# Performance work log

Hardware: AMD Instinct MI355X
Metric: run time of the kernel (lower is better)

The kernel has to match this reference:

```python
import jax, jax.numpy as jnp
import numpy as np

B, N, D = 4, 1024, 1024
T_ITER = 4
E_TYPES = 4  # edge_type_num; module loops over E_TYPES+1 with bitmask
ALPHA = 0.2


def _lin_w(key, out_f, in_f):
    # fan-avg uniform init from custom Linear
    bound = float(np.sqrt(3.0 / ((in_f + out_f) / 2.0)))
    return jax.random.uniform(key, (out_f, in_f), minval=-bound, maxval=bound, dtype=jnp.float32)


def setup_inputs() -> dict:
    key = jax.random.key(0)
    ks = jax.random.split(key, 32)
    inp = {}
    inp['ents'] = jax.random.normal(ks[0], (B, N, D), jnp.float32)
    inp['ent_mask'] = jnp.ones((B, N), jnp.float32)
    inp['q_encoding'] = jax.random.normal(ks[1], (B, D), jnp.float32)
    inp['adj'] = jax.random.randint(ks[2], (B, N, N), 0, E_TYPES + 1, dtype=jnp.int32)
    inp['types'] = 30  # bits 1..4 set -> edge types 1..4 active
    inp['init_mem'] = jax.random.normal(ks[3], (1, D), jnp.float32)
    inp['w_qin'] = _lin_w(ks[4], D, D); inp['b_qin'] = jnp.zeros((D,), jnp.float32)
    inp['w_qt'] = jnp.stack([_lin_w(ks[5 + t], D, D) for t in range(T_ITER)])
    inp['b_qt'] = jnp.zeros((T_ITER, D), jnp.float32)
    inp['w_pl'] = _lin_w(ks[9], D, D);  inp['b_pl'] = jnp.zeros((D,), jnp.float32)
    inp['w_pc'] = _lin_w(ks[10], D, D); inp['b_pc'] = jnp.zeros((D,), jnp.float32)
    inp['w_q'] = _lin_w(ks[11], D, 3 * D); inp['b_q'] = jnp.zeros((D,), jnp.float32)
    inp['w_k'] = _lin_w(ks[12], D, 3 * D); inp['b_k'] = jnp.zeros((D,), jnp.float32)
    inp['w_v'] = _lin_w(ks[13], D, 3 * D); inp['b_v'] = jnp.zeros((D,), jnp.float32)
    inp['w_pk'] = _lin_w(ks[14], D, D); inp['b_pk'] = jnp.zeros((D,), jnp.float32)
    inp['w_pv'] = _lin_w(ks[15], D, D); inp['b_pv'] = jnp.zeros((D,), jnp.float32)
    # wes: xavier_uniform(gain=1.414) on shape (2D, 1); stored flat as (E_TYPES, 2D)
    wb = 1.414 * float(np.sqrt(6.0 / (2 * D + 1)))
    inp['wes'] = jax.random.uniform(ks[16], (E_TYPES, 2 * D), minval=-wb, maxval=wb, dtype=jnp.float32)
    inp['w_mu'] = _lin_w(ks[17], D, 2 * D); inp['b_mu'] = jnp.zeros((D,), jnp.float32)
    inp['w_cb'] = _lin_w(ks[18], D, 2 * D); inp['b_cb'] = jnp.zeros((D,), jnp.float32)
    return inp


def _lin(x, w, b):
    return x @ w.T + b


def _qdgat_forward(ents, ent_mask, q_encoding, adj, types, init_mem,
                   w_qin, b_qin, w_qt, b_qt, w_pl, b_pl, w_pc, b_pc,
                   w_q, b_q, w_k, b_k, w_v, b_v, w_pk, b_pk, w_pv, b_pv,
                   wes, w_mu, b_mu, w_cb, b_cb):
    d = ents.shape[-1]
    x_loc = ents
    x_ctx = jnp.broadcast_to(init_mem, ents.shape)
    # eval mode: var-drop mask is ones scaled by ent_mask
    var_drop = ent_mask[:, :, None]
    adj_pos = adj > 0
    q_base = jax.nn.elu(_lin(q_encoding, w_qin, b_qin))
    n_types = wes.shape[0] + 1  # self.edge_type_num = edge_type_num + 1
    for t in range(T_ITER):
        cmd = _lin(q_base, w_qt[t], b_qt[t])                      # [B,D]
        xc = x_ctx * var_drop
        pl = _lin(x_loc, w_pl, b_pl)
        pc = _lin(xc, w_pc, b_pc)
        x_joint = jnp.concatenate([x_loc, xc, pl * pc], axis=-1)   # [B,N,3D]
        q = _lin(x_joint, w_q, b_q)                               # [B,N,D]
        k = _lin(x_joint, w_k, b_k) * _lin(cmd, w_pk, b_pk)[:, None, :]
        v = _lin(x_joint, w_v, b_v) * _lin(cmd, w_pv, b_pv)[:, None, :]
        # edge_score[b,i,j] = sum over active types T of (adj==T) * (q_i . we[:D] + k_j . we[D:])
        # equivalent to matmul((cat(q_i,k_j) * (adj==T)), we) without materializing [B,N,N,2D]
        edge_score = jnp.zeros(adj.shape, jnp.float32)
        for i in range(n_types):
            if (types >> i) & 1 == 1:
                w1, w2 = wes[i - 1, :d], wes[i - 1, d:]  # i=0 aliases wes[-1], as in torch
                s = (q @ w1)[:, :, None] + (k @ w2)[:, None, :]    # [B,N,N]
                edge_score = edge_score + jnp.where(adj == i, s, 0.0)
        e = jnp.where(edge_score > 0, edge_score, ALPHA * edge_score)  # leaky relu
        logits = jnp.where(adj_pos, e, jnp.float32(-9e15))
        prob = jax.nn.softmax(logits, axis=-1)                     # [B,N,N]
        message = jnp.einsum('bij,bjd->bid', prob, v)
        x_ctx = _lin(jnp.concatenate([xc, message], axis=-1), w_mu, b_mu)
    return _lin(jnp.concatenate([x_loc, x_ctx], axis=-1), w_cb, b_cb)


def reference(ents, ent_mask, q_encoding, adj, types, init_mem,
              w_qin, b_qin, w_qt, b_qt, w_pl, b_pl, w_pc, b_pc,
              w_q, b_q, w_k, b_k, w_v, b_v, w_pk, b_pk, w_pv, b_pv,
              wes, w_mu, b_mu, w_cb, b_cb):
    return _qdgat_forward(ents, ent_mask, q_encoding, adj, types, init_mem,
                          w_qin, b_qin, w_qt, b_qt, w_pl, b_pl, w_pc, b_pc,
                          w_q, b_q, w_k, b_k, w_v, b_v, w_pk, b_pk, w_pv, b_pv,
                          wes, w_mu, b_mu, w_cb, b_cb)
```

## Files before the change

kernel.cpp:

```cpp
#include <hip/hip_runtime.h>
#include <hip/hip_bf16.h>
#include <stdint.h>
#include <stddef.h>


typedef __hip_bfloat16 bf16;
typedef __attribute__((ext_vector_type(8))) short short8;
typedef __attribute__((ext_vector_type(4))) float floatx4;

#define NB 4
#define NN 1024
#define DD 1024
#define NT_ITER 4
#define MM (NB * NN)

static __device__ __forceinline__ float b2f(bf16 x) { return __bfloat162float(x); }
static __device__ __forceinline__ bf16 f2b(float x) { return __float2bfloat16(x); }
static __device__ __forceinline__ unsigned short f2bu(float x) {
    bf16 h = __float2bfloat16(x);
    unsigned short u;
    __builtin_memcpy(&u, &h, 2);
    return u;
}
static __device__ __forceinline__ float bu2f(unsigned short u) {
    unsigned int t = (unsigned int)u << 16;
    float f;
    __builtin_memcpy(&f, &t, 4);
    return f;
}

static __device__ __forceinline__ void gl_lds16(const void* g, void* l) {
    __builtin_amdgcn_global_load_lds(
        (const __attribute__((address_space(1))) unsigned int*)g,
        (__attribute__((address_space(3))) unsigned int*)l, 16, 0, 0);
}

template <int N>
static __device__ __forceinline__ void s_wait_vmcnt() {
    if constexpr (N == 0)      asm volatile("s_waitcnt vmcnt(0)" ::: "memory");
    else if constexpr (N == 4) asm volatile("s_waitcnt vmcnt(4)" ::: "memory");
    else if constexpr (N == 6) asm volatile("s_waitcnt vmcnt(6)" ::: "memory");
    else if constexpr (N == 8) asm volatile("s_waitcnt vmcnt(8)" ::: "memory");
}

__global__ void k_f2b(const float* __restrict__ src, bf16* __restrict__ dst, int n4) {
    int i = blockIdx.x * 256 + threadIdx.x;
    if (i >= n4) return;
    float4 v = ((const float4*)src)[i];
    ushort4 o;
    o.x = f2bu(v.x); o.y = f2bu(v.y); o.z = f2bu(v.z); o.w = f2bu(v.w);
    ((ushort4*)dst)[i] = o;
}

__global__ void k_transw(const float* __restrict__ src, bf16* __restrict__ dst) {
    __shared__ float tile[32][33];
    int c0 = blockIdx.x * 32;
    int r0 = blockIdx.y * 32;
    int tx = threadIdx.x, ty = threadIdx.y;
    for (int i = 0; i < 32; i += 8)
        tile[ty + i][tx] = src[(size_t)(r0 + ty + i) * 3072 + c0 + tx];
    __syncthreads();
    for (int i = 0; i < 32; i += 8)
        dst[(size_t)(c0 + ty + i) * 1024 + r0 + tx] = f2b(tile[tx][ty + i]);
}

__global__ void k_build_sc(const float* __restrict__ pk, const float* __restrict__ wes,
                           bf16* __restrict__ Aq, bf16* __restrict__ Ak) {
    int i = blockIdx.x * 256 + threadIdx.x;
    int half = i >> 16;
    int j = i & 65535;
    int row = j >> 10, d = j & 1023;
    if (half == 0) {
        Aq[j] = (row < 4) ? f2b(wes[(size_t)row * 2048 + d]) : f2b(0.f);
    } else {
        int t = row >> 4, b = (row >> 2) & 3, e = row & 3;
        Ak[j] = f2b(pk[((size_t)t * NB + b) * DD + d] * wes[(size_t)e * 2048 + 1024 + d]);
    }
}

__global__ __launch_bounds__(256) void k_qbase(const float* __restrict__ qenc, const float* __restrict__ w,
                                               const float* __restrict__ b, float* __restrict__ out) {
    int o = blockIdx.x * 4 + (threadIdx.x >> 6);
    int lane = threadIdx.x & 63;
    int n = o >> 2, r = o & 3;
    const float* xr = qenc + (size_t)r * DD;
    const float* wr = w + (size_t)n * DD;
    float s = 0.f;
    for (int d = lane; d < DD; d += 64) s += xr[d] * wr[d];
    for (int off = 32; off; off >>= 1) s += __shfl_down(s, off);
    if (lane == 0) {
        s += b[n];
        out[(size_t)r * DD + n] = s > 0.f ? s : (expf(s) - 1.0f);
    }
}

__global__ __launch_bounds__(256) void k_cmd(const float* __restrict__ qb, const float* __restrict__ w_qt,
                                             const float* __restrict__ b_qt, float* __restrict__ cmd) {
    int o = blockIdx.x * 4 + (threadIdx.x >> 6);
    int lane = threadIdx.x & 63;
    int r = o & 3, n = (o >> 2) & 1023, t = o >> 12;
    const float* xr = qb + (size_t)r * DD;
    const float* wr = w_qt + ((size_t)t * DD + n) * DD;
    float s = 0.f;
    for (int d = lane; d < DD; d += 64) s += xr[d] * wr[d];
    for (int off = 32; off; off >>= 1) s += __shfl_down(s, off);
    if (lane == 0) cmd[((size_t)t * NB + r) * DD + n] = s + b_qt[t * DD + n];
}

__global__ __launch_bounds__(256) void k_pkpv(const float* __restrict__ cmd,
                                              const float* __restrict__ w_pk, const float* __restrict__ b_pk,
                                              const float* __restrict__ w_pv, const float* __restrict__ b_pv,
                                              float* __restrict__ pk, float* __restrict__ pv) {
    int o = blockIdx.x * 4 + (threadIdx.x >> 6);
    int lane = threadIdx.x & 63;
    int n = o >> 5, half = (o >> 4) & 1, pair = o & 15;
    const float* xr = cmd + (size_t)pair * DD;
    const float* wr = (half ? w_pv : w_pk) + (size_t)n * DD;
    float s = 0.f;
    for (int d = lane; d < DD; d += 64) s += xr[d] * wr[d];
    for (int off = 32; off; off >>= 1) s += __shfl_down(s, off);
    if (lane == 0)
        (half ? pv : pk)[(size_t)pair * DD + n] = s + (half ? b_pv : b_pk)[n];
}

__global__ void k_consts(const float* __restrict__ b_q, const float* __restrict__ b_k,
                         const float* __restrict__ pk, const float* __restrict__ wes,
                         float* __restrict__ cq, float* __restrict__ ck) {
    int o = blockIdx.x;
    int lane = threadIdx.x;
    float s = 0.f;
    if (o < 4) {
        for (int d = lane; d < 1024; d += 64) s += b_q[d] * wes[(size_t)o * 2048 + d];
    } else {
        int oo = o - 4;
        int t = oo >> 4, b = (oo >> 2) & 3, e = oo & 3;
        for (int d = lane; d < 1024; d += 64)
            s += b_k[d] * pk[((size_t)t * NB + b) * DD + d] * wes[(size_t)e * 2048 + 1024 + d];
    }
    for (int off = 32; off; off >>= 1) s += __shfl_down(s, off);
    if (lane == 0) {
        if (o < 4) cq[o] = s;
        else ck[o - 4] = s;
    }
}

__global__ __launch_bounds__(256) void k_qakb2(const bf16* __restrict__ ents, const bf16* __restrict__ xc,
                                               const bf16* __restrict__ plpc,
                                               const float* __restrict__ wqtw, const float* __restrict__ wkeff_t,
                                               const float* __restrict__ cq, const float* __restrict__ ck_t,
                                               float* __restrict__ qa, float* __restrict__ kb) {
    __shared__ float red[4][8];
    int m = blockIdx.x;
    int b = m >> 10;
    int t = threadIdx.x;
    float aq[4] = {0.f, 0.f, 0.f, 0.f}, ak[4] = {0.f, 0.f, 0.f, 0.f};
    const bf16* rows[3] = {ents + (size_t)m * DD, xc + (size_t)m * DD, plpc + (size_t)m * DD};
#pragma unroll
    for (int c = 0; c < 3; ++c) {
        const bf16* row = rows[c];
        const float* wq = wqtw + c * 1024;
        const float* wk = wkeff_t + (size_t)b * 4 * 3072 + c * 1024;
        for (int d = t; d < 1024; d += 256) {
            float xv = b2f(row[d]);
#pragma unroll
            for (int e = 0; e < 4; ++e) {
                aq[e] += xv * wq[(size_t)e * 3072 + d];
                ak[e] += xv * wk[(size_t)e * 3072 + d];
            }
        }
    }
#pragma unroll
    for (int e = 0; e < 4; ++e) {
        float v = aq[e];
        for (int o = 32; o; o >>= 1) v += __shfl_down(v, o);
        if ((t & 63) == 0) red[t >> 6][e] = v;
        v = ak[e];
        for (int o = 32; o; o >>= 1) v += __shfl_down(v, o);
        if ((t & 63) == 0) red[t >> 6][e + 4] = v;
    }
    __syncthreads();
    if (t < 8) {
        float s = red[0][t] + red[1][t] + red[2][t] + red[3][t];
        if (t < 4) qa[(size_t)m * 4 + t] = s + cq[t];
        else kb[(size_t)m * 4 + (t - 4)] = s + ck_t[b * 4 + (t - 4)];
    }
}

__global__ void k_init(const bf16* __restrict__ initm_bf, const float* __restrict__ mask,
                       bf16* __restrict__ x_ctx, bf16* __restrict__ xc) {
    int i = blockIdx.x * 256 + threadIdx.x;
    uint4 v = ((const uint4*)initm_bf)[i & 127];
    ((uint4*)x_ctx)[i] = v;
    float mk = mask[i >> 7];
    unsigned short* u = (unsigned short*)&v;
#pragma unroll
    for (int j = 0; j < 8; ++j) u[j] = f2bu(bu2f(u[j]) * mk);
    ((uint4*)xc)[i] = v;
}

template <int WM, int WN>
__device__ __forceinline__ void gemm_core(
    const bf16* __restrict__ A0, const bf16* __restrict__ A1, const bf16* __restrict__ A2,
    const bf16* __restrict__ W, const float* __restrict__ bias, void* __restrict__ C,
    const void* __restrict__ mul, const float* __restrict__ addC, bf16* __restrict__ C2,
    int mulmode, int storef32, int nchunks, int ldw, int ldc,
    int bm, int bn) {
    constexpr int BM = WM * 2;
    constexpr int BN = WN * 2;
    constexpr int MI = WM / 16;
    constexpr int NI = WN / 16;
    constexpr int SEGS = (BM + BN) / 8;
    constexpr int SPW = SEGS / 4;
    __shared__ bf16 sAB[3][(BM + BN) * 64];

    const int t = threadIdx.x;
    const int lane = t & 63;
    const int w = t >> 6;
    const int wm = (w & 1) * WM, wn = (w >> 1) * WN;
    const int srow = lane >> 3;
    const int scol = ((lane & 7) * 8) ^ (srow << 3);

    floatx4 acc[MI][NI];
#pragma unroll
    for (int i = 0; i < MI; ++i)
#pragma unroll
        for (int j = 0; j < NI; ++j) acc[i][j] = (floatx4){0.f, 0.f, 0.f, 0.f};

    const int lrow = lane & 15;
    const int kq = (lane >> 4) * 8;
    const int kx = (lane & 7) << 3;
    const int ktiles = nchunks * 16;

    auto stage = [&](int buf, int kt) {
        const int cidx = kt >> 4;
        const bf16* Ac = (cidx == 0) ? A0 : (cidx == 1 ? A1 : A2);
        const int klocal = (kt & 15) * 64;
        const int kglob = kt * 64;
#pragma unroll
        for (int s = 0; s < SPW; ++s) {
            int c = w * SPW + s;
            if (c < BM / 8) {
                const bf16* src = Ac + ((size_t)(bm * BM + c * 8 + srow)) * 1024 + klocal + scol;
                gl_lds16(src, &sAB[buf][c * 512]);
            } else {
                const bf16* src = W + ((size_t)(bn * BN + (c - BM / 8) * 8 + srow)) * (size_t)ldw + kglob + scol;
                gl_lds16(src, &sAB[buf][c * 512]);
            }
        }
    };

    stage(0, 0);
    if (ktiles > 1) stage(1, 1);
    int cur = 0, sb = 2;
    for (int kt = 0; kt < ktiles; ++kt) {
        if (kt + 1 < ktiles) s_wait_vmcnt<SPW>();
        else s_wait_vmcnt<0>();
        __builtin_amdgcn_s_barrier();
        __builtin_amdgcn_sched_barrier(0);
        short8 af[2][MI], bfr[2][NI];
#pragma unroll
        for (int ks = 0; ks < 2; ++ks) {
            const int ko = (ks * 32 + kq) ^ kx;
#pragma unroll
            for (int mi = 0; mi < MI; ++mi)
                af[ks][mi] = *(const short8*)&sAB[cur][(wm + mi * 16 + lrow) * 64 + ko];
#pragma unroll
            for (int ni = 0; ni < NI; ++ni)
                bfr[ks][ni] = *(const short8*)&sAB[cur][BM * 64 + (wn + ni * 16 + lrow) * 64 + ko];
        }
        if (kt + 2 < ktiles) stage(sb, kt + 2);
        __builtin_amdgcn_s_setprio(1);
#pragma unroll
        for (int ks = 0; ks < 2; ++ks)
#pragma unroll
            for (int mi = 0; mi < MI; ++mi)
#pragma unroll
                for (int ni = 0; ni < NI; ++ni)
                    acc[mi][ni] = __builtin_amdgcn_mfma_f32_16x16x32_bf16(af[ks][mi], bfr[ks][ni], acc[mi][ni], 0, 0, 0);
        __builtin_amdgcn_s_setprio(0);
        asm volatile("s_waitcnt lgkmcnt(0)" ::: "memory");
        __builtin_amdgcn_sched_barrier(0);
        cur = (cur == 2) ? 0 : cur + 1;
        sb = (sb == 2) ? 0 : sb + 1;
    }

    const int qrow = (lane >> 4) * 4;
#pragma unroll
    for (int mi = 0; mi < MI; ++mi) {
#pragma unroll
        for (int ni = 0; ni < NI; ++ni) {
            int gn = bn * BN + wn + ni * 16 + lrow;
            float bv = bias ? bias[gn] : 0.f;
#pragma unroll
            for (int r = 0; r < 4; ++r) {
                int gm = bm * BM + wm + mi * 16 + qrow + r;
                size_t ci = (size_t)gm * (size_t)ldc + gn;
                float val = acc[mi][ni][r] + bv;
                if (addC) val += addC[ci];
                if (mulmode == 1)
                    val *= b2f(((const bf16*)mul)[(size_t)gm * 1024 + gn]);
                else if (mulmode == 2)
                    val *= ((const float*)mul)[(size_t)(gm >> 10) * 1024 + gn];
                if (storef32) {
                    ((float*)C)[ci] = val;
                } else {
                    ((bf16*)C)[ci] = f2b(val);
                    if (mulmode == 3)
                        C2[ci] = f2b(val * ((const float*)mul)[gm]);
                }
            }
        }
    }
}

template <int WM, int WN>
__global__ __launch_bounds__(256) void k_gemm_t(
    const bf16* __restrict__ A0, const bf16* __restrict__ A1, const bf16* __restrict__ A2,
    const bf16* __restrict__ W, const float* __restrict__ bias, void* __restrict__ C,
    const void* __restrict__ mul, const float* __restrict__ addC, bf16* __restrict__ C2,
    int mulmode, int storef32, int nchunks, int ldw, int ldc,
    long long sA, long long sW, long long sC) {
    int bz = blockIdx.z;
    const bf16* A0b = A0 + (size_t)bz * sA;
    const bf16* Wb = W + (size_t)bz * sW;
    void* Cb = storef32 ? (void*)((float*)C + (size_t)bz * sC)
                        : (void*)((bf16*)C + (size_t)bz * sC);
    gemm_core<WM, WN>(A0b, A1, A2, Wb, bias, Cb, mul, addC, C2, mulmode, storef32, nchunks, ldw, ldc,
                      blockIdx.x, blockIdx.y);
}

__global__ void k_transpose(const bf16* __restrict__ v, bf16* __restrict__ vT) {
    __shared__ bf16 tile[32][33];
    int b = blockIdx.z;
    int n0 = blockIdx.x * 32, d0 = blockIdx.y * 32;
    int tx = threadIdx.x, ty = threadIdx.y;
    for (int i = 0; i < 32; i += 8)
        tile[ty + i][tx] = v[((size_t)b * NN + n0 + ty + i) * DD + d0 + tx];
    __syncthreads();
    for (int i = 0; i < 32; i += 8)
        vT[((size_t)b * DD + d0 + ty + i) * NN + n0 + tx] = tile[tx][ty + i];
}

__global__ __launch_bounds__(256) void k_attn(const int* __restrict__ adj, const float* __restrict__ qa,
                                              const float* __restrict__ kb, const int* __restrict__ typesPtr,
                                              bf16* __restrict__ prob) {
    __shared__ float lg[NN];
    __shared__ float red[4];
    __shared__ float red2[4];
    int m = blockIdx.x;
    int b = m >> 10;
    int t = threadIdx.x;
    int types = typesPtr[0];
    float qa4[4];
#pragma unroll
    for (int e = 0; e < 4; ++e) qa4[e] = qa[(size_t)m * 4 + e];
    const int* arow = adj + (size_t)m * NN;
    const float* kbb = kb + (size_t)(b << 10) * 4;

    float lmax = -3.0e38f;
    for (int j = t; j < NN; j += 256) {
        int a = arow[j];
        float l;
        if (a == 0) {
            l = -9.0e15f;
        } else if ((types >> a) & 1) {
            float s = qa4[a - 1] + kbb[(size_t)j * 4 + (a - 1)];
            l = s > 0.f ? s : 0.2f * s;
        } else {
            l = 0.f;
        }
        lg[j] = l;
        lmax = fmaxf(lmax, l);
    }
    for (int o = 32; o > 0; o >>= 1) lmax = fmaxf(lmax, __shfl_down(lmax, o));
    if ((t & 63) == 0) red[t >> 6] = lmax;
    __syncthreads();
    lmax = fmaxf(fmaxf(red[0], red[1]), fmaxf(red[2], red[3]));

    float lsum = 0.f;
    for (int j = t; j < NN; j += 256) {
        float ex = __expf(lg[j] - lmax);
        lg[j] = ex;
        lsum += ex;
    }
    for (int o = 32; o > 0; o >>= 1) lsum += __shfl_down(lsum, o);
    if ((t & 63) == 0) red2[t >> 6] = lsum;
    __syncthreads();
    lsum = red2[0] + red2[1] + red2[2] + red2[3];
    float inv = 1.0f / lsum;

    bf16* prow = prob + (size_t)m * NN;
    for (int j = t; j < NN; j += 256) prow[j] = f2b(lg[j] * inv);
}

extern "C" void kernel_launch(void* const* d_in, const int* in_sizes, int n_in,
                              void* d_out, int out_size, void* d_ws, size_t ws_size,
                              hipStream_t stream) {
    const float* ents = (const float*)d_in[0];
    const float* mask = (const float*)d_in[1];
    const float* qenc = (const float*)d_in[2];
    const int* adj = (const int*)d_in[3];
    const int* types = (const int*)d_in[4];
    const float* initm = (const float*)d_in[5];
    const float* w_qin = (const float*)d_in[6];
    const float* b_qin = (const float*)d_in[7];
    const float* w_qt = (const float*)d_in[8];
    const float* b_qt = (const float*)d_in[9];
    const float* w_pl = (const float*)d_in[10];
    const float* b_pl = (const float*)d_in[11];
    const float* w_pc = (const float*)d_in[12];
    const float* b_pc = (const float*)d_in[13];
    const float* w_q = (const float*)d_in[14];
    const float* b_q = (const float*)d_in[15];
    const float* w_k = (const float*)d_in[16];
    const float* b_k = (const float*)d_in[17];
    const float* w_v = (const float*)d_in[18];
    const float* b_v = (const float*)d_in[19];
    const float* w_pk = (const float*)d_in[20];
    const float* b_pk = (const float*)d_in[21];
    const float* w_pv = (const float*)d_in[22];
    const float* b_pv = (const float*)d_in[23];
    const float* wes = (const float*)d_in[24];
    const float* w_mu = (const float*)d_in[25];
    const float* b_mu = (const float*)d_in[26];
    const float* w_cb = (const float*)d_in[27];
    const float* b_cb = (const float*)d_in[28];
    (void)in_sizes; (void)n_in; (void)out_size; (void)ws_size;

    char* p = (char*)d_ws;
    auto carve = [&](size_t bytes) {
        char* r = p;
        p += (bytes + 255) & ~(size_t)255;
        return r;
    };
    float* q_base = (float*)carve((size_t)NB * DD * 4);
    float* cmd = (float*)carve((size_t)NT_ITER * NB * DD * 4);
    float* pk = (float*)carve((size_t)NT_ITER * NB * DD * 4);
    float* pv = (float*)carve((size_t)NT_ITER * NB * DD * 4);
    float* qa = (float*)carve((size_t)MM * 4 * 4);
    float* kb = (float*)carve((size_t)MM * 4 * 4);
    float* wqtw = (float*)carve((size_t)64 * 3072 * 4);
    float* wkeff = (float*)carve((size_t)64 * 3072 * 4);
    float* cq = (float*)carve(4 * 4);
    float* ck = (float*)carve(64 * 4);
    float* vent = (float*)carve((size_t)MM * DD * 4);
    bf16* initm_bf = (bf16*)carve((size_t)DD * 2);
    bf16* ents_bf = (bf16*)carve((size_t)MM * DD * 2);
    bf16* wpl_bf = (bf16*)carve((size_t)DD * DD * 2);
    bf16* wpc_bf = (bf16*)carve((size_t)DD * DD * 2);
    bf16* wv_bf = (bf16*)carve((size_t)DD * 3 * DD * 2);
    bf16* wmu_bf = (bf16*)carve((size_t)DD * 2 * DD * 2);
    bf16* wcb_bf = (bf16*)carve((size_t)DD * 2 * DD * 2);
    bf16* wqT_bf = (bf16*)carve((size_t)3 * DD * DD * 2);
    bf16* wkT_bf = (bf16*)carve((size_t)3 * DD * DD * 2);
    bf16* Aq = (bf16*)carve((size_t)64 * DD * 2);
    bf16* Ak = (bf16*)carve((size_t)64 * DD * 2);
    bf16* x_ctx = (bf16*)carve((size_t)MM * DD * 2);
    bf16* xc = (bf16*)carve((size_t)MM * DD * 2);
    bf16* pl = (bf16*)carve((size_t)MM * DD * 2);
    bf16* plpc = (bf16*)carve((size_t)MM * DD * 2);
    bf16* vbuf = (bf16*)carve((size_t)MM * DD * 2);
    bf16* msg = (bf16*)carve((size_t)MM * DD * 2);
    bf16* prob = (bf16*)carve((size_t)NB * NN * NN * 2);
    bf16* vT = plpc;

    const dim3 blk(256);
    const dim3 g128(32, 8, 1);
    const dim3 gMsg(8, 8, NB);
    const dim3 gPre(1, 48, 1);

    k_f2b<<<1, blk, 0, stream>>>(initm, initm_bf, DD / 4);
    k_f2b<<<4096, blk, 0, stream>>>(ents, ents_bf, MM * DD / 4);
    k_f2b<<<1024, blk, 0, stream>>>(w_pl, wpl_bf, DD * DD / 4);
    k_f2b<<<1024, blk, 0, stream>>>(w_pc, wpc_bf, DD * DD / 4);
    k_f2b<<<3072, blk, 0, stream>>>(w_v, wv_bf, DD * 3 * DD / 4);
    k_f2b<<<2048, blk, 0, stream>>>(w_mu, wmu_bf, DD * 2 * DD / 4);
    k_f2b<<<2048, blk, 0, stream>>>(w_cb, wcb_bf, DD * 2 * DD / 4);
    k_transw<<<dim3(96, 32), dim3(32, 8), 0, stream>>>(w_q, wqT_bf);
    k_transw<<<dim3(96, 32), dim3(32, 8), 0, stream>>>(w_k, wkT_bf);

    k_qbase<<<1024, blk, 0, stream>>>(qenc, w_qin, b_qin, q_base);
    k_cmd<<<4096, blk, 0, stream>>>(q_base, w_qt, b_qt, cmd);
    k_pkpv<<<8192, blk, 0, stream>>>(cmd, w_pk, b_pk, w_pv, b_pv, pk, pv);
    k_init<<<2048, blk, 0, stream>>>(initm_bf, mask, x_ctx, xc);

    k_build_sc<<<512, blk, 0, stream>>>(pk, wes, Aq, Ak);
    k_consts<<<68, 64, 0, stream>>>(b_q, b_k, pk, wes, cq, ck);
    k_gemm_t<32, 32><<<gPre, blk, 0, stream>>>(Aq, nullptr, nullptr, wqT_bf, nullptr, wqtw,
                                               nullptr, nullptr, nullptr, 0, 1, 1, 1024, 3072, 0, 0, 0);
    k_gemm_t<32, 32><<<gPre, blk, 0, stream>>>(Ak, nullptr, nullptr, wkT_bf, nullptr, wkeff,
                                               nullptr, nullptr, nullptr, 0, 1, 1, 1024, 3072, 0, 0, 0);

    k_gemm_t<64, 64><<<g128, blk, 0, stream>>>(ents_bf, nullptr, nullptr, wpl_bf, b_pl, pl,
                                               nullptr, nullptr, nullptr, 0, 0, 1, 1024, 1024, 0, 0, 0);
    k_gemm_t<64, 64><<<g128, blk, 0, stream>>>(ents_bf, nullptr, nullptr, wv_bf, nullptr, vent,
                                               nullptr, nullptr, nullptr, 0, 1, 1, 3072, 1024, 0, 0, 0);

    for (int t = 0; t < NT_ITER; ++t) {
        k_gemm_t<64, 64><<<g128, blk, 0, stream>>>(xc, nullptr, nullptr, wpc_bf, b_pc, plpc,
                                                   pl, nullptr, nullptr, 1, 0, 1, 1024, 1024, 0, 0, 0);
        k_gemm_t<64, 64><<<g128, blk, 0, stream>>>(xc, plpc, nullptr, wv_bf + 1024, b_v, vbuf,
                                                   pv + (size_t)t * NB * DD, vent, nullptr, 2, 0, 2, 3072, 1024, 0, 0, 0);
        k_qakb2<<<4096, blk, 0, stream>>>(ents_bf, xc, plpc,
                                          wqtw, wkeff + (size_t)t * 16 * 3072,
                                          cq, ck + t * 16, qa, kb);
        k_transpose<<<dim3(32, 32, NB), dim3(32, 8), 0, stream>>>(vbuf, vT);
        k_attn<<<4096, blk, 0, stream>>>(adj, qa, kb, types, prob);
        k_gemm_t<64, 64><<<gMsg, blk, 0, stream>>>(prob, nullptr, nullptr, vT, nullptr, msg,
                                                   nullptr, nullptr, nullptr, 0, 0, 1, 1024, 1024,
                                                   (long long)NN * NN, (long long)DD * NN, (long long)NN * DD);
        k_gemm_t<64, 64><<<g128, blk, 0, stream>>>(xc, msg, nullptr, wmu_bf, b_mu, x_ctx,
                                                   mask, nullptr, xc, 3, 0, 2, 2048, 1024, 0, 0, 0);
    }
    k_gemm_t<64, 64><<<g128, blk, 0, stream>>>(ents_bf, x_ctx, nullptr, wcb_bf, b_cb, (float*)d_out,
                                               nullptr, nullptr, nullptr, 0, 1, 2, 2048, 1024, 0, 0, 0);
}
```

Before: 1.075 ms.

## Replace LDS-tiled GEMM with direct global-to-register double-buffered MFMA GEMM

```diff
diff --git a/kernel.cpp b/kernel.cpp
--- a/kernel.cpp
+++ b/kernel.cpp
@@ -196,6 +196,104 @@
 #pragma unroll
     for (int j = 0; j < 8; ++j) u[j] = f2bu(bu2f(u[j]) * mk);
     ((uint4*)xc)[i] = v;
+}
+
+struct Frags {
+    short8 a[8];
+    short8 b[8];
+};
+
+__global__ __launch_bounds__(256, 1) void k_gemm_d(
+    const bf16* __restrict__ A0, const bf16* __restrict__ A1, const bf16* __restrict__ A2,
+    const bf16* __restrict__ W, const float* __restrict__ bias, void* __restrict__ C,
+    const void* __restrict__ mul, const float* __restrict__ addC, bf16* __restrict__ C2,
+    int mulmode, int storef32, int nchunks, int ldw, int ldc,
+    long long sA, long long sW, long long sC) {
+    const int bz = blockIdx.z;
+    const bf16* A0b = A0 + (size_t)bz * sA;
+    const bf16* Wb = W + (size_t)bz * sW;
+
+    const int t = threadIdx.x;
+    const int lane = t & 63;
+    const int w = t >> 6;
+    const int lrow = lane & 15;
+    const int kq = (lane >> 4) * 8;
+    const int arow = blockIdx.x * 128 + (w & 1) * 64 + lrow;
+    const int wrow = blockIdx.y * 128 + (w >> 1) * 64 + lrow;
+    const int ktiles = nchunks * 16;
+
+    floatx4 acc[4][4];
+#pragma unroll
+    for (int i = 0; i < 4; ++i)
+#pragma unroll
+        for (int j = 0; j < 4; ++j) acc[i][j] = (floatx4){0.f, 0.f, 0.f, 0.f};
+
+    auto loadF = [&](Frags& f, int kt) {
+        const int cidx = kt >> 4;
+        const bf16* Ac = (cidx == 0) ? A0b : (cidx == 1 ? A1 : A2);
+        const bf16* Ab = Ac + (size_t)arow * 1024 + (kt & 15) * 64 + kq;
+        const bf16* Wp = Wb + (size_t)wrow * (size_t)ldw + (size_t)kt * 64 + kq;
+#pragma unroll
+        for (int ks = 0; ks < 2; ++ks) {
+#pragma unroll
+            for (int mi = 0; mi < 4; ++mi)
+                f.a[ks * 4 + mi] = *(const short8*)(Ab + (size_t)mi * 16 * 1024 + ks * 32);
+#pragma unroll
+            for (int ni = 0; ni < 4; ++ni)
+                f.b[ks * 4 + ni] = *(const short8*)(Wp + (size_t)ni * 16 * (size_t)ldw + ks * 32);
+        }
+    };
+    auto mfmaF = [&](const Frags& f) {
+#pragma unroll
+        for (int ks = 0; ks < 2; ++ks)
+#pragma unroll
+            for (int mi = 0; mi < 4; ++mi)
+#pragma unroll
+                for (int ni = 0; ni < 4; ++ni)
+                    acc[mi][ni] = __builtin_amdgcn_mfma_f32_16x16x32_bf16(
+                        f.a[ks * 4 + mi], f.b[ks * 4 + ni], acc[mi][ni], 0, 0, 0);
+    };
+
+    Frags f0, f1;
+    loadF(f0, 0);
+    loadF(f1, 1);
+    int kt = 0;
+    for (; kt < ktiles - 2; kt += 2) {
+        mfmaF(f0);
+        loadF(f0, kt + 2);
+        mfmaF(f1);
+        loadF(f1, kt + 3);
+    }
+    mfmaF(f0);
+    mfmaF(f1);
+
+    const int qrow = (lane >> 4) * 4;
+#pragma unroll
+    for (int mi = 0; mi < 4; ++mi) {
+#pragma unroll
+        for (int ni = 0; ni < 4; ++ni) {
+            int gn = blockIdx.y * 128 + (w >> 1) * 64 + ni * 16 + lrow;
+            float bv = bias ? bias[gn] : 0.f;
+#pragma unroll
+            for (int r = 0; r < 4; ++r) {
+                int gm = blockIdx.x * 128 + (w & 1) * 64 + mi * 16 + qrow + r;
+                size_t ci = (size_t)gm * (size_t)ldc + gn;
+                float val = acc[mi][ni][r] + bv;
+                if (addC) val += addC[ci];
+                if (mulmode == 1)
+                    val *= b2f(((const bf16*)mul)[(size_t)gm * 1024 + gn]);
+                else if (mulmode == 2)
+                    val *= ((const float*)mul)[(size_t)(gm >> 10) * 1024 + gn];
+                if (storef32) {
+                    ((float*)C + (size_t)bz * sC)[ci] = val;
+                } else {
+                    ((bf16*)C + (size_t)bz * sC)[ci] = f2b(val);
+                    if (mulmode == 3)
+                        C2[ci] = f2b(val * ((const float*)mul)[gm]);
+                }
+            }
+        }
+    }
 }
 
 template <int WM, int WN>
@@ -465,7 +563,7 @@
     bf16* vT = plpc;
 
     const dim3 blk(256);
-    const dim3 g128(32, 8, 1);
+    const dim3 gD(32, 8, 1);
     const dim3 gMsg(8, 8, NB);
     const dim3 gPre(1, 48, 1);
 
@@ -491,27 +589,27 @@
     k_gemm_t<32, 32><<<gPre, blk, 0, stream>>>(Ak, nullptr, nullptr, wkT_bf, nullptr, wkeff,
                                                nullptr, nullptr, nullptr, 0, 1, 1, 1024, 3072, 0, 0, 0);
 
-    k_gemm_t<64, 64><<<g128, blk, 0, stream>>>(ents_bf, nullptr, nullptr, wpl_bf, b_pl, pl,
-                                               nullptr, nullptr, nullptr, 0, 0, 1, 1024, 1024, 0, 0, 0);
-    k_gemm_t<64, 64><<<g128, blk, 0, stream>>>(ents_bf, nullptr, nullptr, wv_bf, nullptr, vent,
-                                               nullptr, nullptr, nullptr, 0, 1, 1, 3072, 1024, 0, 0, 0);
+    k_gemm_d<<<gD, blk, 0, stream>>>(ents_bf, nullptr, nullptr, wpl_bf, b_pl, pl,
+                                     nullptr, nullptr, nullptr, 0, 0, 1, 1024, 1024, 0, 0, 0);
+    k_gemm_d<<<gD, blk, 0, stream>>>(ents_bf, nullptr, nullptr, wv_bf, nullptr, vent,
+                                     nullptr, nullptr, nullptr, 0, 1, 1, 3072, 1024, 0, 0, 0);
 
     for (int t = 0; t < NT_ITER; ++t) {
-        k_gemm_t<64, 64><<<g128, blk, 0, stream>>>(xc, nullptr, nullptr, wpc_bf, b_pc, plpc,
-                                                   pl, nullptr, nullptr, 1, 0, 1, 1024, 1024, 0, 0, 0);
-        k_gemm_t<64, 64><<<g128, blk, 0, stream>>>(xc, plpc, nullptr, wv_bf + 1024, b_v, vbuf,
-                                                   pv + (size_t)t * NB * DD, vent, nullptr, 2, 0, 2, 3072, 1024, 0, 0, 0);
+        k_gemm_d<<<gD, blk, 0, stream>>>(xc, nullptr, nullptr, wpc_bf, b_pc, plpc,
+                                         pl, nullptr, nullptr, 1, 0, 1, 1024, 1024, 0, 0, 0);
+        k_gemm_d<<<gD, blk, 0, stream>>>(xc, plpc, nullptr, wv_bf + 1024, b_v, vbuf,
+                                         pv + (size_t)t * NB * DD, vent, nullptr, 2, 0, 2, 3072, 1024, 0, 0, 0);
         k_qakb2<<<4096, blk, 0, stream>>>(ents_bf, xc, plpc,
                                           wqtw, wkeff + (size_t)t * 16 * 3072,
                                           cq, ck + t * 16, qa, kb);
         k_transpose<<<dim3(32, 32, NB), dim3(32, 8), 0, stream>>>(vbuf, vT);
         k_attn<<<4096, blk, 0, stream>>>(adj, qa, kb, types, prob);
-        k_gemm_t<64, 64><<<gMsg, blk, 0, stream>>>(prob, nullptr, nullptr, vT, nullptr, msg,
-                                                   nullptr, nullptr, nullptr, 0, 0, 1, 1024, 1024,
-                                                   (long long)NN * NN, (long long)DD * NN, (long long)NN * DD);
-        k_gemm_t<64, 64><<<g128, blk, 0, stream>>>(xc, msg, nullptr, wmu_bf, b_mu, x_ctx,
-                                                   mask, nullptr, xc, 3, 0, 2, 2048, 1024, 0, 0, 0);
-    }
-    k_gemm_t<64, 64><<<g128, blk, 0, stream>>>(ents_bf, x_ctx, nullptr, wcb_bf, b_cb, (float*)d_out,
-                                               nullptr, nullptr, nullptr, 0, 1, 2, 2048, 1024, 0, 0, 0);
-}
+        k_gemm_d<<<gMsg, blk, 0, stream>>>(prob, nullptr, nullptr, vT, nullptr, msg,
+                                           nullptr, nullptr, nullptr, 0, 0, 1, 1024, 1024,
+                                           (long long)NN * NN, (long long)DD * NN, (long long)NN * DD);
+        k_gemm_d<<<gD, blk, 0, stream>>>(xc, msg, nullptr, wmu_bf, b_mu, x_ctx,
+                                         mask, nullptr, xc, 3, 0, 2, 2048, 1024, 0, 0, 0);
+    }
+    k_gemm_d<<<gD, blk, 0, stream>>>(ents_bf, x_ctx, nullptr, wcb_bf, b_cb, (float*)d_out,
+                                     nullptr, nullptr, nullptr, 0, 1, 2, 2048, 1024, 0, 0, 0);
+}
```

Result: slower. 1.565 ms (+45.6%).
